# Kernel tuning notes

Hardware: AMD Instinct MI355X
Metric: run time of the kernel (lower is better)

Reference implementation:

```python
import jax, jax.numpy as jnp
import numpy as np

N, D, E, EDGE_DIM = 8192, 256, 262144, 1


def setup_inputs() -> dict:
    key = jax.random.key(0)
    ks = jax.random.split(key, 8)
    mag = jax.random.uniform(ks[0], (N, D), dtype=jnp.float32)
    phase = jax.random.normal(ks[1], (N, D), dtype=jnp.float32)
    edge_attr = jax.random.uniform(ks[2], (E, EDGE_DIM), dtype=jnp.float32)
    edge_index = jax.random.randint(ks[3], (2, E), 0, N, dtype=jnp.int64)
    h4 = D // 4
    w1 = jax.random.normal(ks[4], (EDGE_DIM, h4), dtype=jnp.float32) / jnp.sqrt(jnp.float32(EDGE_DIM))
    b1 = jnp.zeros((h4,), dtype=jnp.float32)
    w2 = jax.random.normal(ks[5], (h4, 1), dtype=jnp.float32) / jnp.sqrt(jnp.float32(h4))
    b2 = jnp.zeros((1,), dtype=jnp.float32)
    dist_scale = -jnp.ones((), dtype=jnp.float32)  # torch init: -1.0
    return {"mag": mag, "phase": phase, "edge_attr": edge_attr,
            "edge_index": edge_index, "w1": w1, "b1": b1, "w2": w2,
            "b2": b2, "dist_scale": dist_scale}


def reference(mag, phase, edge_attr, edge_index, w1, b1, w2, b2, dist_scale):
    # scores_ij = sum_d |z_i||z_j| cos(theta_i - theta_j) / sqrt(D)
    # cos(a-b) = cos a cos b + sin a sin b  ->  two N x D GEMMs instead of N x N x D broadcast
    d = mag.shape[-1]
    mc = mag * jnp.cos(phase)  # [N, D]
    ms = mag * jnp.sin(phase)  # [N, D]
    scores = (mc @ mc.T + ms @ ms.T) / jnp.sqrt(jnp.float32(d))  # [N, N]
    # edge bias: MLP(edge_attr) + dist_scale * distance, scattered onto (i, j) pairs
    h = jax.nn.silu(edge_attr @ w1 + b1)          # [E, D//4]
    base_bias = (h @ w2 + b2)[:, 0]               # [E]
    bias_vals = base_bias + dist_scale * edge_attr[:, 0]
    scores = scores.at[edge_index[0], edge_index[1]].add(bias_vals)
    attn = jax.nn.softmax(scores, axis=1)         # [N, N]
    new_mag = attn @ mag                          # [N, D]
    new_phase = attn @ phase                      # [N, D]
    return new_mag, new_phase
```

## Files before the change

### kernel.cpp

```cpp
#include <hip/hip_runtime.h>
#include <hip/hip_bf16.h>
#include <stdint.h>

#define N_NODES 8192
#define KK      512
#define EE      262144
#define BMD     128
#define BND     32
#define NCT     64

typedef __attribute__((ext_vector_type(8))) short short8;
typedef __attribute__((ext_vector_type(4))) float f32x4;
typedef __attribute__((ext_vector_type(4))) unsigned int u32x4;

static __device__ __forceinline__ short f2bf(float f) {
  unsigned u = __builtin_bit_cast(unsigned, f);
  u = (u + 0x7FFFu + ((u >> 16) & 1u)) >> 16;
  return (short)u;
}
static __device__ __forceinline__ float bf2f(unsigned short s) {
  unsigned u = ((unsigned)s) << 16;
  return __builtin_bit_cast(float, u);
}

static constexpr size_t OFF_CNT  = 0;
static constexpr size_t OFF_FLAG = OFF_CNT + 32768;
static constexpr size_t OFF_L    = OFF_FLAG + 256;
static constexpr size_t OFF_OUTW = OFF_L + 32768;
static constexpr size_t MEMSET_BYTES = OFF_OUTW + 16777216;
static constexpr size_t OFF_ABF  = MEMSET_BYTES;
static constexpr size_t OFF_WT   = OFF_ABF + 8388608;
static constexpr size_t OFF_RP   = OFF_WT + 8388608;
static constexpr size_t OFF_CUR  = OFF_RP + 33024;
static constexpr size_t OFF_CCOL = OFF_CUR + 32768;
static constexpr size_t OFF_CB   = OFF_CCOL + 1048576;


__global__ void k_A(const float* __restrict__ mag, const float* __restrict__ phase,
                    short* __restrict__ Abf) {
  int g = blockIdx.x * 256 + threadIdx.x;
  int i = g >> 8, d = g & 255;
  float mg = mag[g], ph = phase[g];
  float sn, cs;
  sincosf(ph, &sn, &cs);
  Abf[(size_t)i * 512 + d]       = f2bf(mg * cs);
  Abf[(size_t)i * 512 + 256 + d] = f2bf(mg * sn);
}

__global__ void k_Wt(const float* __restrict__ mag, const float* __restrict__ phase,
                     short* __restrict__ Wt) {
  __shared__ short tt[32][520];
  int ct = blockIdx.x, tid = threadIdx.x;
  for (int h = 0; h < 2; ++h) {
    const float* src = h ? phase : mag;
#pragma unroll
    for (int m = 0; m < 32; ++m) {
      int idx = m * 256 + tid;
      int kl = idx >> 8, c = idx & 255;
      tt[kl][h * 256 + c] = f2bf(src[(size_t)(ct * 32 + kl) * 256 + c]);
    }
  }
  __syncthreads();
  short* dst = Wt + ((size_t)ct << 14);
#pragma unroll
  for (int m = 0; m < 64; ++m) {
    int idx = m * 256 + tid;
    int nt = idx >> 9, kgq = (idx >> 7) & 3, nl = (idx >> 3) & 15, j = idx & 7;
    dst[idx] = tt[kgq * 8 + j][nt * 16 + nl];
  }
}

__global__ void k_detect(const unsigned* __restrict__ p, int* __restrict__ flag) {
  unsigned acc = 0;
  int idx = blockIdx.x * 256 + threadIdx.x;
  for (int t = idx; t < EE / 2; t += 256 * 256) acc |= p[2 * t + 1];
#pragma unroll
  for (int off = 32; off; off >>= 1) acc |= __shfl_xor(acc, off);
  if ((threadIdx.x & 63) == 0 && acc) atomicOr(flag, 1);
}

__device__ __forceinline__ void load_edge(const void* ei, bool is64, int e, int& i, int& j) {
  if (is64) {
    const long long* p = (const long long*)ei;
    i = (int)p[e]; j = (int)p[EE + e];
  } else {
    const int* p = (const int*)ei;
    i = p[e]; j = p[EE + e];
  }
}

__global__ void k_cnt(const void* ei, const int* __restrict__ flag, int* __restrict__ cnt) {
  int e = blockIdx.x * 256 + threadIdx.x;
  bool is64 = (*flag == 0);
  int i, j;
  load_edge(ei, is64, e, i, j);
  atomicAdd(&cnt[i], 1);
}

__global__ void k_scan(const int* __restrict__ cnt, int* __restrict__ row_ptr,
                       int* __restrict__ cursor) {
  __shared__ int part[1024];
  int tid = threadIdx.x;
  int c[8]; int s = 0;
#pragma unroll
  for (int k = 0; k < 8; ++k) { c[k] = cnt[tid * 8 + k]; s += c[k]; }
  part[tid] = s;
  __syncthreads();
  for (int off = 1; off < 1024; off <<= 1) {
    int v = part[tid];
    int add = (tid >= off) ? part[tid - off] : 0;
    __syncthreads();
    part[tid] = v + add;
    __syncthreads();
  }
  int run = part[tid] - s;
#pragma unroll
  for (int k = 0; k < 8; ++k) {
    row_ptr[tid * 8 + k] = run; cursor[tid * 8 + k] = run; run += c[k];
  }
  if (tid == 1023) row_ptr[8192] = run;
}

__global__ void k_scatter(const void* ei, const int* __restrict__ flag,
                          const float* __restrict__ ea,
                          const float* __restrict__ w1, const float* __restrict__ b1,
                          const float* __restrict__ w2, const float* __restrict__ b2,
                          const float* __restrict__ ds,
                          int* __restrict__ cur,
                          int* __restrict__ ccol, float* __restrict__ cbias) {
  int e = blockIdx.x * 256 + threadIdx.x;
  bool is64 = (*flag == 0);
  int i, j;
  load_edge(ei, is64, e, i, j);
  float x = ea[e];
  float acc = 0.f;
#pragma unroll 8
  for (int u = 0; u < 64; ++u) {
    float z = fmaf(x, w1[u], b1[u]);
    acc = fmaf(z / (1.f + __expf(-z)), w2[u], acc);
  }
  float bias = acc + b2[0] + ds[0] * x;
  int pos = atomicAdd(&cur[i], 1);
  ccol[pos] = j;
  cbias[pos] = bias;
}

#define GLD16(g, l) __builtin_amdgcn_global_load_lds( \
    (const __attribute__((address_space(1))) void*)(g), \
    (__attribute__((address_space(3))) void*)(l), 16, 0, 0)

__global__ __launch_bounds__(512, 2) void k_dense(
    const short* __restrict__ Abf, const short* __restrict__ Wt,
    float* __restrict__ outw, float* __restrict__ l_arr) {
  __shared__ __align__(16) short AcB[2][BND * KK];
  __shared__ __align__(16) short WtB[2][KK * BND];
  __shared__ __align__(16) short Pl[BMD * 40];

  const int tid  = threadIdx.x;
  const int lane = tid & 63;
  const int w    = tid >> 6;
  const int rlow = lane & 15;
  const int kg   = lane >> 4;

  const int bid  = blockIdx.x;
  const int sb   = (bid & 7) * 32 + (bid >> 3);
  const int part = sb >> 6;
  const int rb   = sb & 63;
  const int row0 = rb * BMD;
  const int wrow0 = row0 + w * 16;
  const int ct0   = part * NCT;

  short8 afr[16];
  {
    const short* ap = Abf + ((size_t)(wrow0 + rlow) << 9) + (kg << 3);
#pragma unroll
    for (int kb = 0; kb < 16; ++kb) afr[kb] = *(const short8*)(ap + (kb << 5));
  }
  asm volatile("s_waitcnt vmcnt(0)" ::: "memory");

#define STAGE(buf, ct) do { \
    const short* acsrc_ = Abf + ((size_t)(ct) << 14); \
    const short* wtsrc_ = Wt + ((size_t)(ct) << 14); \
    _Pragma("unroll") \
    for (int i_ = 0; i_ < 4; ++i_) { \
      int slot_ = i_ * 512 + tid; \
      int c_ = slot_ >> 6, x_ = slot_ & 63; \
      GLD16(acsrc_ + ((size_t)c_ << 9) + ((x_ ^ (c_ & 7)) << 3), \
            (char*)&AcB[buf][0] + i_ * 8192 + w * 1024); \
      GLD16(wtsrc_ + (size_t)slot_ * 8, \
            (char*)&WtB[buf][0] + i_ * 8192 + w * 1024); \
    } \
  } while (0)

  STAGE(0, ct0 + 0);
  STAGE(1, ct0 + 1);

  const f32x4 zero4 = {0.f, 0.f, 0.f, 0.f};
  f32x4 acc[8][4];
#pragma unroll
  for (int rt = 0; rt < 8; ++rt)
#pragma unroll
    for (int dt = 0; dt < 4; ++dt) acc[rt][dt] = zero4;
  float lac[4] = {0.f, 0.f, 0.f, 0.f};

#pragma unroll 1
  for (int ci = 0; ci < NCT; ++ci) {
    const int cur = ci & 1;
    asm volatile("s_waitcnt vmcnt(8)" ::: "memory");
    __builtin_amdgcn_sched_barrier(0);
    __builtin_amdgcn_s_barrier();
    __builtin_amdgcn_sched_barrier(0);

    const short* ac = &AcB[cur][0];
    f32x4 s0 = zero4, s1 = zero4;
    __builtin_amdgcn_s_setprio(1);
#pragma unroll
    for (int kb = 0; kb < 16; ++kb) {
      int sw = (((kb << 2) + kg) ^ (rlow & 7)) << 3;
      short8 b0 = *(const short8*)(ac + (rlow << 9) + sw);
      short8 b1 = *(const short8*)(ac + ((16 + rlow) << 9) + sw);
      s0 = __builtin_amdgcn_mfma_f32_16x16x32_bf16(afr[kb], b0, s0, 0, 0, 0);
      s1 = __builtin_amdgcn_mfma_f32_16x16x32_bf16(afr[kb], b1, s1, 0, 0, 0);
    }
    __builtin_amdgcn_s_setprio(0);

    float pr[4];
#pragma unroll
    for (int r = 0; r < 4; ++r) {
      float p0 = __expf(s0[r] * 0.0625f);
      float p1 = __expf(s1[r] * 0.0625f);
      pr[r] = p0 + p1;
      int prow = (w << 4) + (kg << 2) + r;
      Pl[prow * 40 + rlow]      = f2bf(p0);
      Pl[prow * 40 + 16 + rlow] = f2bf(p1);
    }
#pragma unroll
    for (int off = 1; off <= 8; off <<= 1) {
#pragma unroll
      for (int r = 0; r < 4; ++r) pr[r] += __shfl_xor(pr[r], off);
    }
#pragma unroll
    for (int r = 0; r < 4; ++r) lac[r] += pr[r];

    asm volatile("s_waitcnt lgkmcnt(0)" ::: "memory");
    __builtin_amdgcn_s_barrier();
    __builtin_amdgcn_sched_barrier(0);

    const short* wt = &WtB[cur][0];
    short8 wtf[4];
#pragma unroll
    for (int dt = 0; dt < 4; ++dt)
      wtf[dt] = *(const short8*)(wt + (((w << 2) + dt) << 9) + (kg << 7) + (rlow << 3));
    __builtin_amdgcn_s_setprio(1);
#pragma unroll
    for (int rt = 0; rt < 8; ++rt) {
      short8 pa = *(const short8*)(&Pl[((rt << 4) + rlow) * 40 + (kg << 3)]);
#pragma unroll
      for (int dt = 0; dt < 4; ++dt)
        acc[rt][dt] = __builtin_amdgcn_mfma_f32_16x16x32_bf16(pa, wtf[dt], acc[rt][dt], 0, 0, 0);
    }
    __builtin_amdgcn_s_setprio(0);

    __builtin_amdgcn_s_barrier();
    __builtin_amdgcn_sched_barrier(0);
    STAGE(cur, ct0 + ((ci + 2) & (NCT - 1)));
  }

#pragma unroll
  for (int rt = 0; rt < 8; ++rt) {
#pragma unroll
    for (int dt = 0; dt < 4; ++dt) {
#pragma unroll
      for (int r = 0; r < 4; ++r) {
        int row = row0 + (rt << 4) + (kg << 2) + r;
        int dim = (w << 6) + (dt << 4) + rlow;
        atomicAdd(&outw[((size_t)row << 9) + dim], acc[rt][dt][r]);
      }
    }
  }
  if (rlow == 0) {
#pragma unroll
    for (int r = 0; r < 4; ++r)
      atomicAdd(&l_arr[wrow0 + (kg << 2) + r], lac[r]);
  }
}
#undef STAGE
#undef GLD16

__global__ __launch_bounds__(256) void k_corr(
    const short* __restrict__ Abf, const float* __restrict__ mag,
    const float* __restrict__ phase, const int* __restrict__ row_ptr,
    const int* __restrict__ ccol, const float* __restrict__ cbias,
    float* __restrict__ outw, float* __restrict__ l_arr) {
  int lane = threadIdx.x & 63;
  int i = blockIdx.x * 4 + (threadIdx.x >> 6);
  int s = row_ptr[i], e = row_ptr[i + 1];
  if (s >= e) return;

  short8 ai = *(const short8*)(Abf + ((size_t)i << 9) + (lane << 3));
  float aif[8];
#pragma unroll
  for (int u = 0; u < 8; ++u) aif[u] = bf2f((unsigned short)ai[u]);

  int myq = s + lane;
  bool have = myq < e;
  int jv = have ? ccol[myq] : -1;
  float bv = have ? cbias[myq] : 0.f;

  float acc[8] = {0.f, 0.f, 0.f, 0.f, 0.f, 0.f, 0.f, 0.f};
  float lacc = 0.f;
  int d0 = lane << 3;
  const float* wbase = (d0 < 256) ? (mag + d0) : (phase + (d0 - 256));

  for (int q = s; q < e; ++q) {
    int qs = q - s;
    int j = (qs < 64) ? __shfl(jv, qs) : ccol[q];
    short8 aj = *(const short8*)(Abf + ((size_t)j << 9) + (lane << 3));
    f32x4 w0 = *(const f32x4*)(wbase + ((size_t)j << 8));
    f32x4 w1 = *(const f32x4*)(wbase + ((size_t)j << 8) + 4);
    float p = 0.f;
#pragma unroll
    for (int u = 0; u < 8; ++u) p = fmaf(aif[u], bf2f((unsigned short)aj[u]), p);
    float bs = (jv == j) ? bv : 0.f;
    int mi = (jv == j) ? myq : 0x7FFFFFFF;
    for (int b2 = s + 64; b2 < e; b2 += 64) {
      int q2 = b2 + lane;
      if (q2 < e && ccol[q2] == j) { bs += cbias[q2]; mi = min(mi, q2); }
    }
#pragma unroll
    for (int off = 32; off; off >>= 1) {
      p  += __shfl_xor(p, off);
      bs += __shfl_xor(bs, off);
      mi  = min(mi, __shfl_xor(mi, off));
    }
    float st = p * 0.0625f;
    float dw = (mi == q) ? (__expf(st + bs) - __expf(st)) : 0.f;
    acc[0] = fmaf(dw, w0[0], acc[0]);
    acc[1] = fmaf(dw, w0[1], acc[1]);
    acc[2] = fmaf(dw, w0[2], acc[2]);
    acc[3] = fmaf(dw, w0[3], acc[3]);
    acc[4] = fmaf(dw, w1[0], acc[4]);
    acc[5] = fmaf(dw, w1[1], acc[5]);
    acc[6] = fmaf(dw, w1[2], acc[6]);
    acc[7] = fmaf(dw, w1[3], acc[7]);
    lacc += dw;
  }
  float* op = outw + ((size_t)i << 9) + d0;
#pragma unroll
  for (int u = 0; u < 8; ++u) op[u] += acc[u];
  if (lane == 0) l_arr[i] += lacc;
}

__global__ void k_norm(const float* __restrict__ o, const float* __restrict__ l_arr,
                       float* __restrict__ out) {
  int g = blockIdx.x * 256 + threadIdx.x;
  int i = g >> 9, d = g & 511;
  float v = o[g] / l_arr[i];
  size_t dst = (d < 256) ? ((size_t)i * 256 + d)
                         : ((size_t)N_NODES * 256 + (size_t)i * 256 + (d - 256));
  out[dst] = v;
}

extern "C" void kernel_launch(void* const* d_in, const int* in_sizes, int n_in,
                              void* d_out, int out_size, void* d_ws, size_t ws_size,
                              hipStream_t stream) {
  const float* mag   = (const float*)d_in[0];
  const float* phase = (const float*)d_in[1];
  const float* ea    = (const float*)d_in[2];
  const void*  ei    = d_in[3];
  const float* w1    = (const float*)d_in[4];
  const float* b1    = (const float*)d_in[5];
  const float* w2    = (const float*)d_in[6];
  const float* b2    = (const float*)d_in[7];
  const float* ds    = (const float*)d_in[8];

  char* ws = (char*)d_ws;
  int*   cnt   = (int*)(ws + OFF_CNT);
  int*   flag  = (int*)(ws + OFF_FLAG);
  float* l_arr = (float*)(ws + OFF_L);
  float* outw  = (float*)(ws + OFF_OUTW);
  short* Abf   = (short*)(ws + OFF_ABF);
  short* Wt    = (short*)(ws + OFF_WT);
  int*   rp    = (int*)(ws + OFF_RP);
  int*   cur   = (int*)(ws + OFF_CUR);
  int*   ccol  = (int*)(ws + OFF_CCOL);
  float* cbias = (float*)(ws + OFF_CB);

  hipMemsetAsync(d_ws, 0, MEMSET_BYTES, stream);
  k_detect<<<256, 256, 0, stream>>>((const unsigned*)ei, flag);
  k_A<<<8192, 256, 0, stream>>>(mag, phase, Abf);
  k_Wt<<<256, 256, 0, stream>>>(mag, phase, Wt);
  k_cnt<<<1024, 256, 0, stream>>>(ei, flag, cnt);
  k_scan<<<1, 1024, 0, stream>>>(cnt, rp, cur);
  k_scatter<<<1024, 256, 0, stream>>>(ei, flag, ea, w1, b1, w2, b2, ds, cur, ccol, cbias);
  k_dense<<<256, 512, 0, stream>>>(Abf, Wt, outw, l_arr);
  k_corr<<<2048, 256, 0, stream>>>(Abf, mag, phase, rp, ccol, cbias, outw, l_arr);
  k_norm<<<16384, 256, 0, stream>>>(outw, l_arr, (float*)d_out);
  (void)in_sizes; (void)n_in; (void)out_size; (void)ws_size;
}
```

Before: 525.4 us.

## Load W tiles directly to registers, defer row-sum reduction, restructure edge-correction kernel

The dense kernel stops staging the value matrix Wt through LDS. Each wave now loads its W fragments straight from global memory at the start of each chunk, which halves the LDS footprint and the async copy count. The next A stage is issued earlier, removing one barrier per iteration, the P tile stride is shrunk, and the row-sum shuffle reduction moves out of the loop to the end. The edge-correction kernel adds a fast path for rows with at most 64 edges: duplicate detection and dot products are done once per edge, weight rows are loaded only for edges with nonzero delta, and output updates are vectorized. The trade-off is that direct global W loads may stall the MFMA phase if latency is not hidden.

```diff
diff --git a/kernel.cpp b/kernel.cpp
--- a/kernel.cpp
+++ b/kernel.cpp
@@ -10,6 +10,7 @@
 #define NCT     64
 
 typedef __attribute__((ext_vector_type(8))) short short8;
+typedef __attribute__((ext_vector_type(4))) short short4_t;
 typedef __attribute__((ext_vector_type(4))) float f32x4;
 typedef __attribute__((ext_vector_type(4))) unsigned int u32x4;
 
@@ -153,8 +154,7 @@
     const short* __restrict__ Abf, const short* __restrict__ Wt,
     float* __restrict__ outw, float* __restrict__ l_arr) {
   __shared__ __align__(16) short AcB[2][BND * KK];
-  __shared__ __align__(16) short WtB[2][KK * BND];
-  __shared__ __align__(16) short Pl[BMD * 40];
+  __shared__ __align__(16) short Pl[BMD * 36];
 
   const int tid  = threadIdx.x;
   const int lane = tid & 63;
@@ -180,15 +180,12 @@
 
 #define STAGE(buf, ct) do { \
     const short* acsrc_ = Abf + ((size_t)(ct) << 14); \
-    const short* wtsrc_ = Wt + ((size_t)(ct) << 14); \
     _Pragma("unroll") \
     for (int i_ = 0; i_ < 4; ++i_) { \
       int slot_ = i_ * 512 + tid; \
       int c_ = slot_ >> 6, x_ = slot_ & 63; \
       GLD16(acsrc_ + ((size_t)c_ << 9) + ((x_ ^ (c_ & 7)) << 3), \
             (char*)&AcB[buf][0] + i_ * 8192 + w * 1024); \
-      GLD16(wtsrc_ + (size_t)slot_ * 8, \
-            (char*)&WtB[buf][0] + i_ * 8192 + w * 1024); \
     } \
   } while (0)
 
@@ -206,10 +203,17 @@
 #pragma unroll 1
   for (int ci = 0; ci < NCT; ++ci) {
     const int cur = ci & 1;
-    asm volatile("s_waitcnt vmcnt(8)" ::: "memory");
+    const int ct  = ct0 + ci;
+    asm volatile("s_waitcnt vmcnt(4)" ::: "memory");
     __builtin_amdgcn_sched_barrier(0);
     __builtin_amdgcn_s_barrier();
     __builtin_amdgcn_sched_barrier(0);
+
+    const short* wtg = Wt + ((size_t)ct << 14) + (((size_t)w << 11)) + (kg << 7) + (rlow << 3);
+    short8 wtf0 = *(const short8*)(wtg);
+    short8 wtf1 = *(const short8*)(wtg + 512);
+    short8 wtf2 = *(const short8*)(wtg + 1024);
+    short8 wtf3 = *(const short8*)(wtg + 1536);
 
     const short* ac = &AcB[cur][0];
     f32x4 s0 = zero4, s1 = zero4;
@@ -224,48 +228,47 @@
     }
     __builtin_amdgcn_s_setprio(0);
 
-    float pr[4];
 #pragma unroll
     for (int r = 0; r < 4; ++r) {
       float p0 = __expf(s0[r] * 0.0625f);
       float p1 = __expf(s1[r] * 0.0625f);
-      pr[r] = p0 + p1;
+      lac[r] += p0 + p1;
       int prow = (w << 4) + (kg << 2) + r;
-      Pl[prow * 40 + rlow]      = f2bf(p0);
-      Pl[prow * 40 + 16 + rlow] = f2bf(p1);
-    }
-#pragma unroll
-    for (int off = 1; off <= 8; off <<= 1) {
-#pragma unroll
-      for (int r = 0; r < 4; ++r) pr[r] += __shfl_xor(pr[r], off);
-    }
-#pragma unroll
-    for (int r = 0; r < 4; ++r) lac[r] += pr[r];
+      Pl[prow * 36 + rlow]      = f2bf(p0);
+      Pl[prow * 36 + 16 + rlow] = f2bf(p1);
+    }
 
     asm volatile("s_waitcnt lgkmcnt(0)" ::: "memory");
     __builtin_amdgcn_s_barrier();
     __builtin_amdgcn_sched_barrier(0);
 
-    const short* wt = &WtB[cur][0];
-    short8 wtf[4];
-#pragma unroll
-    for (int dt = 0; dt < 4; ++dt)
-      wtf[dt] = *(const short8*)(wt + (((w << 2) + dt) << 9) + (kg << 7) + (rlow << 3));
+    STAGE(cur, ct0 + ((ci + 2) & (NCT - 1)));
+
     __builtin_amdgcn_s_setprio(1);
 #pragma unroll
     for (int rt = 0; rt < 8; ++rt) {
-      short8 pa = *(const short8*)(&Pl[((rt << 4) + rlow) * 40 + (kg << 3)]);
-#pragma unroll
-      for (int dt = 0; dt < 4; ++dt)
-        acc[rt][dt] = __builtin_amdgcn_mfma_f32_16x16x32_bf16(pa, wtf[dt], acc[rt][dt], 0, 0, 0);
+      const short* pb = &Pl[((rt << 4) + rlow) * 36 + (kg << 3)];
+      short4_t pl0 = *(const short4_t*)(pb);
+      short4_t pl1 = *(const short4_t*)(pb + 4);
+      short8 pa = {pl0[0], pl0[1], pl0[2], pl0[3], pl1[0], pl1[1], pl1[2], pl1[3]};
+      acc[rt][0] = __builtin_amdgcn_mfma_f32_16x16x32_bf16(pa, wtf0, acc[rt][0], 0, 0, 0);
+      acc[rt][1] = __builtin_amdgcn_mfma_f32_16x16x32_bf16(pa, wtf1, acc[rt][1], 0, 0, 0);
+      acc[rt][2] = __builtin_amdgcn_mfma_f32_16x16x32_bf16(pa, wtf2, acc[rt][2], 0, 0, 0);
+      acc[rt][3] = __builtin_amdgcn_mfma_f32_16x16x32_bf16(pa, wtf3, acc[rt][3], 0, 0, 0);
     }
     __builtin_amdgcn_s_setprio(0);
-
-    __builtin_amdgcn_s_barrier();
-    __builtin_amdgcn_sched_barrier(0);
-    STAGE(cur, ct0 + ((ci + 2) & (NCT - 1)));
-  }
-
+  }
+
+#pragma unroll
+  for (int off = 1; off <= 8; off <<= 1) {
+#pragma unroll
+    for (int r = 0; r < 4; ++r) lac[r] += __shfl_xor(lac[r], off);
+  }
+  if (rlow == 0) {
+#pragma unroll
+    for (int r = 0; r < 4; ++r)
+      atomicAdd(&l_arr[wrow0 + (kg << 2) + r], lac[r]);
+  }
 #pragma unroll
   for (int rt = 0; rt < 8; ++rt) {
 #pragma unroll
@@ -277,11 +280,6 @@
         atomicAdd(&outw[((size_t)row << 9) + dim], acc[rt][dt][r]);
       }
     }
-  }
-  if (rlow == 0) {
-#pragma unroll
-    for (int r = 0; r < 4; ++r)
-      atomicAdd(&l_arr[wrow0 + (kg << 2) + r], lac[r]);
   }
 }
 #undef STAGE
@@ -295,59 +293,94 @@
   int lane = threadIdx.x & 63;
   int i = blockIdx.x * 4 + (threadIdx.x >> 6);
   int s = row_ptr[i], e = row_ptr[i + 1];
-  if (s >= e) return;
+  int len = e - s;
+  if (len <= 0) return;
 
   short8 ai = *(const short8*)(Abf + ((size_t)i << 9) + (lane << 3));
   float aif[8];
 #pragma unroll
   for (int u = 0; u < 8; ++u) aif[u] = bf2f((unsigned short)ai[u]);
 
-  int myq = s + lane;
-  bool have = myq < e;
-  int jv = have ? ccol[myq] : -1;
-  float bv = have ? cbias[myq] : 0.f;
-
-  float acc[8] = {0.f, 0.f, 0.f, 0.f, 0.f, 0.f, 0.f, 0.f};
+  f32x4 acc0 = {0.f, 0.f, 0.f, 0.f}, acc1 = {0.f, 0.f, 0.f, 0.f};
   float lacc = 0.f;
   int d0 = lane << 3;
   const float* wbase = (d0 < 256) ? (mag + d0) : (phase + (d0 - 256));
 
-  for (int q = s; q < e; ++q) {
-    int qs = q - s;
-    int j = (qs < 64) ? __shfl(jv, qs) : ccol[q];
-    short8 aj = *(const short8*)(Abf + ((size_t)j << 9) + (lane << 3));
-    f32x4 w0 = *(const f32x4*)(wbase + ((size_t)j << 8));
-    f32x4 w1 = *(const f32x4*)(wbase + ((size_t)j << 8) + 4);
-    float p = 0.f;
-#pragma unroll
-    for (int u = 0; u < 8; ++u) p = fmaf(aif[u], bf2f((unsigned short)aj[u]), p);
-    float bs = (jv == j) ? bv : 0.f;
-    int mi = (jv == j) ? myq : 0x7FFFFFFF;
-    for (int b2 = s + 64; b2 < e; b2 += 64) {
-      int q2 = b2 + lane;
-      if (q2 < e && ccol[q2] == j) { bs += cbias[q2]; mi = min(mi, q2); }
-    }
-#pragma unroll
-    for (int off = 32; off; off >>= 1) {
-      p  += __shfl_xor(p, off);
-      bs += __shfl_xor(bs, off);
-      mi  = min(mi, __shfl_xor(mi, off));
-    }
-    float st = p * 0.0625f;
-    float dw = (mi == q) ? (__expf(st + bs) - __expf(st)) : 0.f;
-    acc[0] = fmaf(dw, w0[0], acc[0]);
-    acc[1] = fmaf(dw, w0[1], acc[1]);
-    acc[2] = fmaf(dw, w0[2], acc[2]);
-    acc[3] = fmaf(dw, w0[3], acc[3]);
-    acc[4] = fmaf(dw, w1[0], acc[4]);
-    acc[5] = fmaf(dw, w1[1], acc[5]);
-    acc[6] = fmaf(dw, w1[2], acc[6]);
-    acc[7] = fmaf(dw, w1[3], acc[7]);
-    lacc += dw;
+  if (len <= 64) {
+    int jv = (lane < len) ? ccol[s + lane] : -1;
+    float bvv = (lane < len) ? cbias[s + lane] : 0.f;
+    float bs = 0.f; int mi = 64;
+    for (int t = 0; t < len; ++t) {
+      int c = __shfl(jv, t); float b = __shfl(bvv, t);
+      if (c == jv) { bs += b; mi = min(mi, t); }
+    }
+    float pown = 0.f;
+    for (int t = 0; t < len; ++t) {
+      int j = __shfl(jv, t);
+      short8 aj = *(const short8*)(Abf + ((size_t)j << 9) + (lane << 3));
+      float p = 0.f;
+#pragma unroll
+      for (int u = 0; u < 8; ++u) p = fmaf(aif[u], bf2f((unsigned short)aj[u]), p);
+#pragma unroll
+      for (int off = 32; off; off >>= 1) p += __shfl_xor(p, off);
+      if (lane == t) pown = p;
+    }
+    float dwown = 0.f;
+    if (lane < len && mi == lane) {
+      float st = pown * 0.0625f;
+      dwown = __expf(st + bs) - __expf(st);
+    }
+    for (int t = 0; t < len; ++t) {
+      float dw = __shfl(dwown, t);
+      if (dw != 0.f) {
+        int j = __shfl(jv, t);
+        f32x4 w0 = *(const f32x4*)(wbase + ((size_t)j << 8));
+        f32x4 w1 = *(const f32x4*)(wbase + ((size_t)j << 8) + 4);
+#pragma unroll
+        for (int u = 0; u < 4; ++u) { acc0[u] = fmaf(dw, w0[u], acc0[u]); acc1[u] = fmaf(dw, w1[u], acc1[u]); }
+        lacc += dw;
+      }
+    }
+  } else {
+    int myq = s + lane;
+    bool have = myq < e;
+    int jv = have ? ccol[myq] : -1;
+    float bvv = have ? cbias[myq] : 0.f;
+    for (int q = s; q < e; ++q) {
+      int qs = q - s;
+      int j = (qs < 64) ? __shfl(jv, qs) : ccol[q];
+      short8 aj = *(const short8*)(Abf + ((size_t)j << 9) + (lane << 3));
+      float p = 0.f;
+#pragma unroll
+      for (int u = 0; u < 8; ++u) p = fmaf(aif[u], bf2f((unsigned short)aj[u]), p);
+      float bs = (jv == j) ? bvv : 0.f;
+      int mi = (jv == j) ? myq : 0x7FFFFFFF;
+      for (int b2 = s + 64; b2 < e; b2 += 64) {
+        int q2 = b2 + lane;
+        if (q2 < e && ccol[q2] == j) { bs += cbias[q2]; mi = min(mi, q2); }
+      }
+#pragma unroll
+      for (int off = 32; off; off >>= 1) {
+        p  += __shfl_xor(p, off);
+        bs += __shfl_xor(bs, off);
+        mi  = min(mi, __shfl_xor(mi, off));
+      }
+      float st = p * 0.0625f;
+      float dw = (mi == q) ? (__expf(st + bs) - __expf(st)) : 0.f;
+      f32x4 w0 = *(const f32x4*)(wbase + ((size_t)j << 8));
+      f32x4 w1 = *(const f32x4*)(wbase + ((size_t)j << 8) + 4);
+#pragma unroll
+      for (int u = 0; u < 4; ++u) { acc0[u] = fmaf(dw, w0[u], acc0[u]); acc1[u] = fmaf(dw, w1[u], acc1[u]); }
+      lacc += dw;
+    }
   }
   float* op = outw + ((size_t)i << 9) + d0;
-#pragma unroll
-  for (int u = 0; u < 8; ++u) op[u] += acc[u];
+  f32x4 o0 = *(const f32x4*)(op);
+  f32x4 o1 = *(const f32x4*)(op + 4);
+#pragma unroll
+  for (int u = 0; u < 4; ++u) { o0[u] += acc0[u]; o1[u] += acc1[u]; }
+  *(f32x4*)(op)     = o0;
+  *(f32x4*)(op + 4) = o1;
   if (lane == 0) l_arr[i] += lacc;
 }
 
```

New measurement: 470.3 us. -10.5%, faster.
